# Kernel optimization log

Hardware: AMD Instinct MI355X
Metric: run time of the kernel (lower is better)

The kernel has to match this reference:

```python
import jax, jax.numpy as jnp
import numpy as np

L, E, H, FFE = 4, 512, 8, 512  # layers, embed, heads, ff dim (must equal E for residual)
HD = E // H


def _ln(x, g, b):
    mu = jnp.mean(x, -1, keepdims=True)
    var = jnp.mean((x - mu) ** 2, -1, keepdims=True)
    return (x - mu) / jnp.sqrt(var + 1e-5) * g + b


def setup_inputs() -> dict:
    key = jax.random.key(0)
    ks = jax.random.split(key, 8)
    B, S = 8, 128
    w = lambda k, shape: jax.random.normal(k, shape, jnp.float32) * 0.02
    return {
        "x": jax.random.normal(ks[0], (B, S, E), jnp.float32),
        "Wq": w(ks[1], (L, E, E)), "bq": jnp.zeros((L, E), jnp.float32),
        "Wk": w(ks[2], (L, E, E)), "bk": jnp.zeros((L, E), jnp.float32),
        "Wv": w(ks[3], (L, E, E)), "bv": jnp.zeros((L, E), jnp.float32),
        "Wo": w(ks[4], (L, E, E)), "bo": jnp.zeros((L, E), jnp.float32),
        "Wf": w(ks[5], (L, E, FFE)), "bf": jnp.zeros((L, FFE), jnp.float32),
        "g1": jnp.ones((L, E), jnp.float32), "b1": jnp.zeros((L, E), jnp.float32),
        "g2": jnp.ones((L, FFE), jnp.float32), "b2": jnp.zeros((L, FFE), jnp.float32),
    }


def reference(x, Wq, bq, Wk, bk, Wv, bv, Wo, bo, Wf, bf, g1, b1, g2, b2):
    B, S, _ = x.shape

    def stack(xb, mask):
        # xb: [B,S,E]; mask: [S] bool, True = key position inside current prefix.
        # Non-causal MHA restricted to prefix keys exactly reproduces running
        # the original stack on x[:, :s, :] (query positions beyond the prefix
        # produce values we never read).
        h = xb
        for l in range(L):
            q = (h @ Wq[l] + bq[l]).reshape(B, S, H, HD)
            k = (h @ Wk[l] + bk[l]).reshape(B, S, H, HD)
            v = (h @ Wv[l] + bv[l]).reshape(B, S, H, HD)
            sc = jnp.einsum('bqhd,bkhd->bhqk', q, k) / jnp.sqrt(jnp.float32(HD))
            sc = jnp.where(mask[None, None, None, :], sc, jnp.float32(-1e9))
            a = jax.nn.softmax(sc, axis=-1)
            o = jnp.einsum('bhqk,bkhd->bqhd', a, v).reshape(B, S, E)
            h = _ln(o @ Wo[l] + bo[l] + h, g1[l], b1[l])          # MHA + residual + LN1
            h = _ln(jax.nn.relu(h @ Wf[l] + bf[l]) + h, g2[l], b2[l])  # FF + ReLU + residual + LN2
        return h

    # masks[s-1] selects keys 0..s-1 -> prefix of length s
    masks = jnp.tril(jnp.ones((S, S), bool))
    outs = jax.vmap(stack, in_axes=(None, 0))(x, masks)  # [S, B, S, E]
    idx = jnp.arange(S)
    last = outs[idx, :, idx]  # [S, B, E]: last valid token of each prefix run
    return jnp.transpose(last, (1, 0, 2))  # [B, S, E]
```

## Files before the change

### kernel.cpp

```cpp
#include <hip/hip_runtime.h>
#include <stdint.h>

typedef unsigned short u16;
typedef __attribute__((ext_vector_type(8))) short bf16x8;
typedef __attribute__((ext_vector_type(4))) float f32x4;

#define EE 512
#define NH 8
#define HDm 64
#define SS 128
#define NB 8
#define NL 4
#define QKVW 1536

__device__ __forceinline__ float bf2f(u16 v){ union{uint32_t u; float f;} c; c.u=((uint32_t)v)<<16; return c.f; }
__device__ __forceinline__ u16 f2bf(float f){ union{float f; uint32_t u;} c; c.f=f; uint32_t u=c.u; return (u16)((u + 0x7FFFu + ((u>>16)&1u))>>16); }

__device__ __forceinline__ f32x4 mfma16(bf16x8 a, bf16x8 b, f32x4 c){
  return __builtin_amdgcn_mfma_f32_16x16x32_bf16(a,b,c,0,0,0);
}

__device__ __forceinline__ void gload16(const u16* g, u16* l){
  auto gp = reinterpret_cast<const __attribute__((address_space(1))) uint32_t*>(reinterpret_cast<uintptr_t>(g));
  auto lp = reinterpret_cast<__attribute__((address_space(3))) uint32_t*>(reinterpret_cast<uintptr_t>(l));
  __builtin_amdgcn_global_load_lds(gp, lp, 16, 0, 0);
}

#define ABAR() asm volatile("s_barrier" ::: "memory")
#define SB0()  __builtin_amdgcn_sched_barrier(0)

__device__ __forceinline__ void run_map(int bid, int cb, int U, int& r, int& u){
  int rr = 0;
  for (;;){
    int g = (cb + rr) >> 4;
    int gend = ((g + 1) << 4) - cb;
    int upr = (g + 1) * U;
    int span = (gend - rr) * upr;
    if (bid < span){ r = rr + bid / upr; u = bid % upr; return; }
    bid -= span; rr = gend;
  }
}

__global__ __launch_bounds__(256) void prep(const float* __restrict__ Wq, const float* __restrict__ Wk,
                                            const float* __restrict__ Wv, const float* __restrict__ Wo,
                                            const float* __restrict__ Wf,
                                            const float* __restrict__ bq, const float* __restrict__ bk,
                                            const float* __restrict__ bv, const float* __restrict__ x,
                                            u16* __restrict__ WqkvT, u16* __restrict__ WoT,
                                            u16* __restrict__ WfT, float* __restrict__ bqkv,
                                            u16* __restrict__ h0){
  int bid = blockIdx.x;
  int t = threadIdx.x;
  if (bid < 5120){
    __shared__ float tl[32][33];
    int grp = bid >> 10;
    int within = bid & 1023;
    int l = within >> 8, tile = within & 255;
    const float* W; u16* dst; int dstL, dstOff;
    switch(grp){
      case 0: W=Wq; dst=WqkvT; dstL=QKVW*EE; dstOff=0;    break;
      case 1: W=Wk; dst=WqkvT; dstL=QKVW*EE; dstOff=512;  break;
      case 2: W=Wv; dst=WqkvT; dstL=QKVW*EE; dstOff=1024; break;
      case 3: W=Wo; dst=WoT;   dstL=EE*EE;   dstOff=0;    break;
      default:W=Wf; dst=WfT;   dstL=EE*EE;   dstOff=0;    break;
    }
    int ot = tile & 15, it = tile >> 4;
    int c = t & 31, r = t >> 5;
    #pragma unroll
    for (int k=0;k<4;k++){
      int ri = it*32 + r + k*8;
      tl[c][r + k*8] = W[(size_t)l*262144 + (size_t)ri*512 + ot*32 + c];
    }
    __syncthreads();
    #pragma unroll
    for (int k=0;k<4;k++){
      int ro = ot*32 + r + k*8;
      dst[(size_t)l*dstL + (size_t)(dstOff + ro)*512 + it*32 + c] = f2bf(tl[r + k*8][c]);
    }
  } else if (bid < 5144){
    int i = (bid - 5120)*256 + t;
    int l = i / QKVW, n = i % QKVW;
    const float* b = (n < 512) ? bq : ((n < 1024) ? bk : bv);
    bqkv[i] = b[l*EE + (n & 511)];
  } else {
    int i = ((bid - 5144)*256 + t)*8;
    int e = i & 511;
    int pb = i >> 9;
    int b = pb & 7, pp = pb >> 3;
    const float* xp = x + (((size_t)b*SS + pp)<<9) + e;
    union{ bf16x8 v; u16 u[8]; } rv;
    #pragma unroll
    for (int j=0;j<8;j++) rv.u[j] = f2bf(xp[j]);
    *(bf16x8*)(h0 + i) = rv.v;
  }
}

template<int MODE>
__global__ __launch_bounds__(256) void gemm_bt(const u16* __restrict__ A, const u16* __restrict__ Bt,
                                               const float* __restrict__ bias, const u16* __restrict__ res,
                                               u16* __restrict__ o0, u16* __restrict__ o1, u16* __restrict__ o2,
                                               int cb, size_t res_mask){
  __shared__ u16 As[2][128*64];
  __shared__ u16 Bs[2][128*64];
  int t = threadIdx.x;
  int T = gridDim.x, NY = gridDim.y;
  int tile_idx, yb;
  if ((T & 7) == 0){
    int hw = blockIdx.y * T + blockIdx.x;
    int xcd = hw & 7, u = hw >> 3;
    yb = u % NY;
    tile_idx = (u / NY) * 8 + xcd;
  } else { tile_idx = blockIdx.x; yb = blockIdx.y; }
  size_t m0;
  if (cb < 0){
    m0 = (size_t)tile_idx * 128;
  } else {
    int r, tile; run_map(tile_idx, cb, 1, r, tile);
    m0 = (size_t)r*1024 + (size_t)tile*128;
  }
  int n0 = yb*128;
  int wid=t>>6, lane=t&63;
  int wm=wid>>1, wn=wid&1, lr=lane&15, lq=lane>>4;
  f32x4 acc[4][4] = {};
  int srow = t>>3;
  int cg2 = (t&7) ^ (srow&7);
  const u16* gA = A + (m0+(size_t)srow)*EE + cg2*8;
  const u16* gB = Bt + ((size_t)(n0+srow))*EE + cg2*8;

  auto stage = [&](int kt, int slot){
    int k0 = kt*64;
    u16* lA = As[slot] + t*8;
    u16* lB = Bs[slot] + t*8;
    #pragma unroll
    for (int j=0;j<4;j++){
      gload16(gA + (size_t)j*32*EE + k0, lA + j*2048);
      gload16(gB + (size_t)j*32*EE + k0, lB + j*2048);
    }
  };

  stage(0,0); stage(1,1);

  #pragma unroll
  for (int kt=0; kt<8; kt++){
    int slot = kt & 1;
    if (kt < 7) asm volatile("s_waitcnt vmcnt(8)" ::: "memory");
    else        asm volatile("s_waitcnt vmcnt(0)" ::: "memory");
    ABAR();
    bf16x8 a[4][2], b[4][2];
    #pragma unroll
    for (int mi=0;mi<4;mi++){
      int row = wm*64 + mi*16 + lr;
      #pragma unroll
      for (int kk=0;kk<2;kk++){
        int c = (kk*4 + lq) ^ (row&7);
        a[mi][kk] = *(const bf16x8*)(As[slot] + row*64 + c*8);
      }
    }
    #pragma unroll
    for (int ni=0;ni<4;ni++){
      int row = wn*64 + ni*16 + lr;
      #pragma unroll
      for (int kk=0;kk<2;kk++){
        int c = (kk*4 + lq) ^ (row&7);
        b[ni][kk] = *(const bf16x8*)(Bs[slot] + row*64 + c*8);
      }
    }
    asm volatile("s_waitcnt lgkmcnt(0)" ::: "memory");
    SB0();
    ABAR();
    if (kt < 6) stage(kt+2, slot);
    #pragma unroll
    for (int mi=0;mi<4;mi++)
      #pragma unroll
      for (int ni=0;ni<4;ni++){
        acc[mi][ni] = mfma16(a[mi][0], b[ni][0], acc[mi][ni]);
        acc[mi][ni] = mfma16(a[mi][1], b[ni][1], acc[mi][ni]);
      }
  }

  int g4 = lane>>4;
  u16* outp;
  int nb;
  if (MODE==0){ int sel = n0 >> 9; outp = sel==0 ? o0 : (sel==1 ? o1 : o2); nb = n0 & 511; }
  else        { outp = o0; nb = n0; }
  #pragma unroll
  for (int ni=0;ni<4;ni++){
    int coln = wn*64 + ni*16 + lr;
    float bv = bias[n0 + coln];
    int col = nb + coln;
    #pragma unroll
    for (int mi=0;mi<4;mi++){
      #pragma unroll
      for (int j=0;j<4;j++){
        size_t row = m0 + (size_t)(wm*64 + mi*16 + g4*4 + j);
        float v = acc[mi][ni][j] + bv;
        if (MODE==2) v = fmaxf(v, 0.f);
        if (MODE>=1) v += bf2f(res[(row & res_mask)*EE + col]);
        outp[row*EE + col] = f2bf(v);
      }
    }
  }
}

__global__ __launch_bounds__(256) void attn(const u16* __restrict__ Q, const u16* __restrict__ K,
                                            const u16* __restrict__ V, u16* __restrict__ Oq,
                                            int cb, int shared_qkv){
  __shared__ u16 Ks[128*72];
  __shared__ u16 Vt[64*136];
  __shared__ u16 Ps[4][16*136];
  int t = threadIdx.x;
  int idx = blockIdx.x;
  int hh = idx & 7, b = (idx>>3)&7, r = idx>>6;
  int m_run = cb + r;
  const size_t RS = (size_t)SS*NB*EE;
  size_t rbase = shared_qkv ? 0 : (size_t)r*RS;
  size_t hb = (size_t)b*EE + hh*HDm;
  size_t obase = (size_t)r*RS + hb;
  int nkc = m_run/32 + 1;
  int nkt = nkc*2;
  int nqt = m_run/16 + 1;
  int nkr = nkt*16;
  for (int i=t; i<nkr*8; i+=256){
    int row=i>>3, c=(i&7)*8;
    *(uint4*)(Ks + row*72 + c) = *(const uint4*)(K + rbase + (size_t)row*NB*EE + hb + c);
  }
  for (int i=t; i<nkr*8; i+=256){
    int row=i>>3, c=(i&7)*8;
    uint4 raw = *(const uint4*)(V + rbase + (size_t)row*NB*EE + hb + c);
    const u16* pv = (const u16*)&raw;
    #pragma unroll
    for (int j=0;j<8;j++) Vt[(c+j)*136 + row] = pv[j];
  }
  __syncthreads();
  int wid=t>>6, lane=t&63, lr=lane&15, g=lane>>4, lk=(lane>>4)*8;
  u16* Pw = Ps[wid];
  for (int iq=0; iq<2; iq++){
    int qt = wid*2 + iq;
    if (qt >= nqt) continue;
    const u16* qrow = Q + rbase + (size_t)(qt*16+lr)*NB*EE + hb;
    bf16x8 qa0 = *(const bf16x8*)(qrow + lk);
    bf16x8 qa1 = *(const bf16x8*)(qrow + 32 + lk);
    f32x4 sc[8];
    #pragma unroll
    for (int kt=0;kt<8;kt++){
      if (kt < nkt){
        f32x4 c = {};
        bf16x8 kb0 = *(const bf16x8*)(Ks + (kt*16+lr)*72 + lk);
        bf16x8 kb1 = *(const bf16x8*)(Ks + (kt*16+lr)*72 + 32 + lk);
        c = mfma16(qa0, kb0, c);
        c = mfma16(qa1, kb1, c);
        int key = kt*16 + lr;
        #pragma unroll
        for (int i2=0;i2<4;i2++)
          sc[kt][i2] = (key <= m_run) ? c[i2]*0.125f : -1e9f;
      }
    }
    #pragma unroll
    for (int i2=0;i2<4;i2++){
      float v = -3.0e38f;
      #pragma unroll
      for (int kt=0;kt<8;kt++) if (kt<nkt) v = fmaxf(v, sc[kt][i2]);
      v = fmaxf(v, __shfl_xor(v,1));
      v = fmaxf(v, __shfl_xor(v,2));
      v = fmaxf(v, __shfl_xor(v,4));
      v = fmaxf(v, __shfl_xor(v,8));
      float s = 0.f;
      #pragma unroll
      for (int kt=0;kt<8;kt++) if (kt<nkt){ float e2=__expf(sc[kt][i2]-v); sc[kt][i2]=e2; s+=e2; }
      s += __shfl_xor(s,1); s += __shfl_xor(s,2); s += __shfl_xor(s,4); s += __shfl_xor(s,8);
      float inv = 1.f/s;
      #pragma unroll
      for (int kt=0;kt<8;kt++) if (kt<nkt) sc[kt][i2] *= inv;
    }
    #pragma unroll
    for (int kt=0;kt<8;kt++) if (kt<nkt){
      #pragma unroll
      for (int i2=0;i2<4;i2++)
        Pw[(g*4+i2)*136 + kt*16 + lr] = f2bf(sc[kt][i2]);
    }
    f32x4 oa[4] = {};
    #pragma unroll
    for (int kc=0;kc<4;kc++) if (kc<nkc){
      bf16x8 pa = *(const bf16x8*)(Pw + lr*136 + kc*32 + lk);
      #pragma unroll
      for (int dt=0;dt<4;dt++){
        bf16x8 vb = *(const bf16x8*)(Vt + (dt*16+lr)*136 + kc*32 + lk);
        oa[dt] = mfma16(pa, vb, oa[dt]);
      }
    }
    #pragma unroll
    for (int dt=0;dt<4;dt++){
      #pragma unroll
      for (int j=0;j<4;j++){
        size_t prow = (size_t)(qt*16 + g*4 + j);
        Oq[obase + prow*NB*EE + dt*16 + lr] = f2bf(oa[dt][j]);
      }
    }
  }
}

__global__ __launch_bounds__(256) void lnorm(const u16* __restrict__ in, const float* __restrict__ gg,
                                             const float* __restrict__ bb, u16* __restrict__ outp,
                                             float* __restrict__ fout, int last, int cb){
  int r, u; run_map(blockIdx.x, cb, 8, r, u);
  int lane = threadIdx.x & 63;
  float gv[8], bv2[8];
  #pragma unroll
  for (int j=0;j<8;j++){ gv[j] = gg[lane*8+j]; bv2[j] = bb[lane*8+j]; }
  int m_run = cb + r;
  #pragma unroll
  for (int it=0; it<4; it++){
    int local = u*16 + it*4 + (threadIdx.x>>6);
    size_t row = (size_t)r*1024 + local;
    const u16* p = in + row*EE + lane*8;
    union{ bf16x8 v; u16 u[8]; } d; d.v = *(const bf16x8*)p;
    float f[8]; float s=0.f;
    #pragma unroll
    for (int j=0;j<8;j++){ f[j]=bf2f(d.u[j]); s+=f[j]; }
    #pragma unroll
    for (int o=1;o<64;o<<=1) s += __shfl_xor(s,o);
    float mu = s*(1.f/512.f);
    float s2=0.f;
    #pragma unroll
    for (int j=0;j<8;j++){ float tt=f[j]-mu; s2+=tt*tt; }
    #pragma unroll
    for (int o=1;o<64;o<<=1) s2 += __shfl_xor(s2,o);
    float rstd = rsqrtf(s2*(1.f/512.f)+1e-5f);
    union{ bf16x8 v; u16 u[8]; } rr;
    #pragma unroll
    for (int j=0;j<8;j++) rr.u[j] = f2bf((f[j]-mu)*rstd*gv[j] + bv2[j]);
    *(bf16x8*)(outp + row*EE + lane*8) = rr.v;
    if (last){
      int pidx = local >> 3, b3 = local & 7;
      if (pidx == m_run){
        #pragma unroll
        for (int j=0;j<8;j++) fout[((size_t)b3*SS + pidx)*EE + lane*8 + j] = bf2f(rr.u[j]);
      }
    }
  }
}

extern "C" void kernel_launch(void* const* d_in, const int* in_sizes, int n_in,
                              void* d_out, int out_size, void* d_ws, size_t ws_size,
                              hipStream_t stream){
  const float* x   = (const float*)d_in[0];
  const float* Wq  = (const float*)d_in[1];
  const float* bq  = (const float*)d_in[2];
  const float* Wk  = (const float*)d_in[3];
  const float* bk  = (const float*)d_in[4];
  const float* Wv  = (const float*)d_in[5];
  const float* bv  = (const float*)d_in[6];
  const float* Wo  = (const float*)d_in[7];
  const float* bo  = (const float*)d_in[8];
  const float* Wf  = (const float*)d_in[9];
  const float* bfb = (const float*)d_in[10];
  const float* g1  = (const float*)d_in[11];
  const float* b1  = (const float*)d_in[12];
  const float* g2  = (const float*)d_in[13];
  const float* b2  = (const float*)d_in[14];
  float* out = (float*)d_out;

  uint8_t* p = (uint8_t*)d_ws;
  u16* WqkvT = (u16*)p; p += (size_t)NL*QKVW*EE*2;
  u16* WoT   = (u16*)p; p += (size_t)NL*EE*EE*2;
  u16* WfT   = (u16*)p; p += (size_t)NL*EE*EE*2;
  float* bqkv= (float*)p; p += (size_t)NL*QKVW*4;
  u16* h0    = (u16*)p; p += (size_t)SS*NB*EE*2;
  u16* q0    = (u16*)p; p += (size_t)SS*NB*EE*2;
  u16* k0    = (u16*)p; p += (size_t)SS*NB*EE*2;
  u16* v0    = (u16*)p; p += (size_t)SS*NB*EE*2;
  size_t used = (size_t)(p - (uint8_t*)d_ws);

  int RC = 128;
  const size_t PER_RUN = (size_t)SS*NB*EE*2*5;
  while (RC > 1 && used + (size_t)RC*PER_RUN > ws_size) RC >>= 1;

  const size_t BUF = (size_t)RC*SS*NB*EE*2;
  u16* h   = (u16*)p; p += BUF;
  u16* q   = (u16*)p; p += BUF;
  u16* k   = (u16*)p; p += BUF;
  u16* v   = (u16*)p; p += BUF;
  u16* tmp = (u16*)p; p += BUF;

  const size_t NOMASK = ~(size_t)0;
  const size_t QL = (size_t)QKVW*EE;
  const size_t OL = (size_t)EE*EE;

  prep<<<5400,256,0,stream>>>(Wq, Wk, Wv, Wo, Wf, bq, bk, bv, x, WqkvT, WoT, WfT, bqkv, h0);
  gemm_bt<0><<<dim3(8,12),256,0,stream>>>(h0, WqkvT, bqkv, nullptr, q0, k0, v0, -1, 0);

  for (int cb=0; cb<SS; cb+=RC){
    int t128 = 0;
    for (int r2=0;r2<RC;r2++) t128 += (cb+r2)/16 + 1;

    attn<<<dim3(RC*64),256,0,stream>>>(q0, k0, v0, q, cb, 1);
    gemm_bt<1><<<dim3(t128,4),256,0,stream>>>(q, WoT, bo, h0, tmp, nullptr, nullptr, cb, (size_t)1023);
    lnorm<<<dim3(t128*8),256,0,stream>>>(tmp, g1, b1, h, nullptr, 0, cb);
    gemm_bt<2><<<dim3(t128,4),256,0,stream>>>(h, WfT, bfb, h, tmp, nullptr, nullptr, cb, NOMASK);
    lnorm<<<dim3(t128*8),256,0,stream>>>(tmp, g2, b2, h, nullptr, 0, cb);

    for (int l=1;l<NL;l++){
      gemm_bt<0><<<dim3(t128,12),256,0,stream>>>(h, WqkvT+(size_t)l*QL, bqkv+l*QKVW, nullptr, q, k, v, cb, 0);
      attn<<<dim3(RC*64),256,0,stream>>>(q, k, v, q, cb, 0);
      gemm_bt<1><<<dim3(t128,4),256,0,stream>>>(q, WoT+(size_t)l*OL, bo+l*EE, h, tmp, nullptr, nullptr, cb, NOMASK);
      lnorm<<<dim3(t128*8),256,0,stream>>>(tmp, g1+l*EE, b1+l*EE, h, nullptr, 0, cb);
      gemm_bt<2><<<dim3(t128,4),256,0,stream>>>(h, WfT+(size_t)l*OL, bfb+l*EE, h, tmp, nullptr, nullptr, cb, NOMASK);
      lnorm<<<dim3(t128*8),256,0,stream>>>(tmp, g2+l*EE, b2+l*EE, h, out, (l==NL-1) ? 1 : 0, cb);
    }
  }
}
```

Measured before the change: 1.832 ms.

## Fuse output/FF projection GEMMs with residual add and LayerNorm

Replaces the Wo and Wf GEMMs plus their separate LayerNorm kernels with a single kernel per stage. Each 512-thread block computes a full 64x512 row tile, reduces per-row mean and variance through shuffles and LDS, and writes the normalized bf16 rows and the final float outputs directly. This removes the tmp buffer round-trip and two launches per layer. In exchange it uses larger per-block LDS (80KB dynamic), variance computed as E[x^2]-mu^2 in fp32, and h is read as the residual and written as the output in the same kernel across different blocks' rows.

```diff
diff --git a/kernel.cpp b/kernel.cpp
--- a/kernel.cpp
+++ b/kernel.cpp
@@ -95,11 +95,10 @@
   }
 }
 
-template<int MODE>
-__global__ __launch_bounds__(256) void gemm_bt(const u16* __restrict__ A, const u16* __restrict__ Bt,
-                                               const float* __restrict__ bias, const u16* __restrict__ res,
-                                               u16* __restrict__ o0, u16* __restrict__ o1, u16* __restrict__ o2,
-                                               int cb, size_t res_mask){
+__global__ __launch_bounds__(256) void gemm_qkv(const u16* __restrict__ A, const u16* __restrict__ Bt,
+                                                const float* __restrict__ bias,
+                                                u16* __restrict__ o0, u16* __restrict__ o1, u16* __restrict__ o2,
+                                                int cb){
   __shared__ u16 As[2][128*64];
   __shared__ u16 Bs[2][128*64];
   int t = threadIdx.x;
@@ -179,10 +178,9 @@
   }
 
   int g4 = lane>>4;
-  u16* outp;
-  int nb;
-  if (MODE==0){ int sel = n0 >> 9; outp = sel==0 ? o0 : (sel==1 ? o1 : o2); nb = n0 & 511; }
-  else        { outp = o0; nb = n0; }
+  int sel = n0 >> 9;
+  u16* outp = sel==0 ? o0 : (sel==1 ? o1 : o2);
+  int nb = n0 & 511;
   #pragma unroll
   for (int ni=0;ni<4;ni++){
     int coln = wn*64 + ni*16 + lr;
@@ -193,10 +191,155 @@
       #pragma unroll
       for (int j=0;j<4;j++){
         size_t row = m0 + (size_t)(wm*64 + mi*16 + g4*4 + j);
-        float v = acc[mi][ni][j] + bv;
+        outp[row*EE + col] = f2bf(acc[mi][ni][j] + bv);
+      }
+    }
+  }
+}
+
+template<int MODE>
+__global__ __launch_bounds__(512, 2) void gemm_ln(const u16* __restrict__ A, const u16* __restrict__ Bt,
+                                                  const float* __restrict__ bias, const u16* __restrict__ res,
+                                                  size_t res_mask, const float* __restrict__ lng,
+                                                  const float* __restrict__ lnb, u16* __restrict__ outh,
+                                                  float* __restrict__ fout, int last, int cb){
+  extern __shared__ u16 lds[];
+  u16* Asl = lds;
+  u16* Bsl = lds + 8192;
+  int t = threadIdx.x;
+  int r, u64; run_map(blockIdx.x, cb, 2, r, u64);
+  int m_run = cb + r;
+  size_t m0 = (size_t)r*1024 + (size_t)u64*64;
+  int wid = t>>6, lane = t&63;
+  int lr = lane&15, lq = lane>>4;
+
+  int srow = t>>3;
+  int cg = (t&7) ^ (srow&7);
+  const u16* gA = A + (m0 + (size_t)srow)*EE + cg*8;
+  const u16* gB = Bt + (size_t)srow*EE + cg*8;
+
+  auto stageA = [&](int kt, int slot){
+    gload16(gA + kt*64, Asl + slot*4096 + t*8);
+  };
+  auto stageB = [&](int kt){
+    int k0 = kt*64;
+    #pragma unroll
+    for (int j=0;j<8;j++)
+      gload16(gB + (size_t)j*64*EE + k0, Bsl + (j*512 + t)*8);
+  };
+
+  f32x4 acc[4][4] = {};
+  stageA(0,0); stageB(0); stageA(1,1);
+
+  #pragma unroll
+  for (int kt=0; kt<8; kt++){
+    int slot = kt & 1;
+    if (kt < 7) asm volatile("s_waitcnt vmcnt(1)" ::: "memory");
+    else        asm volatile("s_waitcnt vmcnt(0)" ::: "memory");
+    ABAR();
+    bf16x8 a[4][2], b[4][2];
+    #pragma unroll
+    for (int mi=0;mi<4;mi++){
+      int row = mi*16 + lr;
+      #pragma unroll
+      for (int kk=0;kk<2;kk++){
+        int c = (kk*4 + lq) ^ (row&7);
+        a[mi][kk] = *(const bf16x8*)(Asl + slot*4096 + row*64 + c*8);
+      }
+    }
+    #pragma unroll
+    for (int ni=0;ni<4;ni++){
+      int row = wid*64 + ni*16 + lr;
+      #pragma unroll
+      for (int kk=0;kk<2;kk++){
+        int c = (kk*4 + lq) ^ (row&7);
+        b[ni][kk] = *(const bf16x8*)(Bsl + row*64 + c*8);
+      }
+    }
+    asm volatile("s_waitcnt lgkmcnt(0)" ::: "memory");
+    SB0();
+    ABAR();
+    if (kt < 7) stageB(kt+1);
+    if (kt < 6) stageA(kt+2, slot);
+    #pragma unroll
+    for (int mi=0;mi<4;mi++)
+      #pragma unroll
+      for (int ni=0;ni<4;ni++){
+        acc[mi][ni] = mfma16(a[mi][0], b[ni][0], acc[mi][ni]);
+        acc[mi][ni] = mfma16(a[mi][1], b[ni][1], acc[mi][ni]);
+      }
+  }
+
+  float psum[4][4] = {}, psq[4][4] = {};
+  #pragma unroll
+  for (int ni=0;ni<4;ni++){
+    int col = wid*64 + ni*16 + lr;
+    float bb = bias[col];
+    #pragma unroll
+    for (int mi=0;mi<4;mi++){
+      #pragma unroll
+      for (int j=0;j<4;j++){
+        size_t row = m0 + (size_t)(mi*16 + lq*4 + j);
+        float v = acc[mi][ni][j] + bb;
         if (MODE==2) v = fmaxf(v, 0.f);
-        if (MODE>=1) v += bf2f(res[(row & res_mask)*EE + col]);
-        outp[row*EE + col] = f2bf(v);
+        v += bf2f(res[(row & res_mask)*EE + col]);
+        acc[mi][ni][j] = v;
+        psum[mi][j] += v; psq[mi][j] += v*v;
+      }
+    }
+  }
+  #pragma unroll
+  for (int o=1;o<16;o<<=1){
+    #pragma unroll
+    for (int mi=0;mi<4;mi++)
+      #pragma unroll
+      for (int j=0;j<4;j++){
+        psum[mi][j] += __shfl_xor(psum[mi][j], o);
+        psq[mi][j]  += __shfl_xor(psq[mi][j], o);
+      }
+  }
+  float2* red = (float2*)lds;
+  __syncthreads();
+  if (lr == 0){
+    #pragma unroll
+    for (int mi=0;mi<4;mi++)
+      #pragma unroll
+      for (int j=0;j<4;j++)
+        red[(mi*16 + lq*4 + j)*8 + wid] = make_float2(psum[mi][j], psq[mi][j]);
+  }
+  __syncthreads();
+  float mu_[4][4], rs_[4][4];
+  #pragma unroll
+  for (int mi=0;mi<4;mi++){
+    #pragma unroll
+    for (int j=0;j<4;j++){
+      int row64 = mi*16 + lq*4 + j;
+      float sm = 0.f, sq = 0.f;
+      #pragma unroll
+      for (int k2=0;k2<8;k2++){ float2 e = red[row64*8 + k2]; sm += e.x; sq += e.y; }
+      float mu = sm * (1.f/512.f);
+      float var = sq * (1.f/512.f) - mu*mu;
+      mu_[mi][j] = mu;
+      rs_[mi][j] = rsqrtf(var + 1e-5f);
+    }
+  }
+  #pragma unroll
+  for (int ni=0;ni<4;ni++){
+    int col = wid*64 + ni*16 + lr;
+    float gg = lng[col], bb2 = lnb[col];
+    #pragma unroll
+    for (int mi=0;mi<4;mi++){
+      #pragma unroll
+      for (int j=0;j<4;j++){
+        float vv = (acc[mi][ni][j] - mu_[mi][j]) * rs_[mi][j] * gg + bb2;
+        u16 hb = f2bf(vv);
+        size_t row = m0 + (size_t)(mi*16 + lq*4 + j);
+        outh[row*EE + col] = hb;
+        if (MODE==2 && last){
+          int local = u64*64 + mi*16 + lq*4 + j;
+          int pidx = local >> 3, b3 = local & 7;
+          if (pidx == m_run) fout[((size_t)b3*SS + pidx)*EE + col] = bf2f(hb);
+        }
       }
     }
   }
@@ -299,47 +442,6 @@
   }
 }
 
-__global__ __launch_bounds__(256) void lnorm(const u16* __restrict__ in, const float* __restrict__ gg,
-                                             const float* __restrict__ bb, u16* __restrict__ outp,
-                                             float* __restrict__ fout, int last, int cb){
-  int r, u; run_map(blockIdx.x, cb, 8, r, u);
-  int lane = threadIdx.x & 63;
-  float gv[8], bv2[8];
-  #pragma unroll
-  for (int j=0;j<8;j++){ gv[j] = gg[lane*8+j]; bv2[j] = bb[lane*8+j]; }
-  int m_run = cb + r;
-  #pragma unroll
-  for (int it=0; it<4; it++){
-    int local = u*16 + it*4 + (threadIdx.x>>6);
-    size_t row = (size_t)r*1024 + local;
-    const u16* p = in + row*EE + lane*8;
-    union{ bf16x8 v; u16 u[8]; } d; d.v = *(const bf16x8*)p;
-    float f[8]; float s=0.f;
-    #pragma unroll
-    for (int j=0;j<8;j++){ f[j]=bf2f(d.u[j]); s+=f[j]; }
-    #pragma unroll
-    for (int o=1;o<64;o<<=1) s += __shfl_xor(s,o);
-    float mu = s*(1.f/512.f);
-    float s2=0.f;
-    #pragma unroll
-    for (int j=0;j<8;j++){ float tt=f[j]-mu; s2+=tt*tt; }
-    #pragma unroll
-    for (int o=1;o<64;o<<=1) s2 += __shfl_xor(s2,o);
-    float rstd = rsqrtf(s2*(1.f/512.f)+1e-5f);
-    union{ bf16x8 v; u16 u[8]; } rr;
-    #pragma unroll
-    for (int j=0;j<8;j++) rr.u[j] = f2bf((f[j]-mu)*rstd*gv[j] + bv2[j]);
-    *(bf16x8*)(outp + row*EE + lane*8) = rr.v;
-    if (last){
-      int pidx = local >> 3, b3 = local & 7;
-      if (pidx == m_run){
-        #pragma unroll
-        for (int j=0;j<8;j++) fout[((size_t)b3*SS + pidx)*EE + lane*8 + j] = bf2f(rr.u[j]);
-      }
-    }
-  }
-}
-
 extern "C" void kernel_launch(void* const* d_in, const int* in_sizes, int n_in,
                               void* d_out, int out_size, void* d_ws, size_t ws_size,
                               hipStream_t stream){
@@ -360,6 +462,9 @@
   const float* b2  = (const float*)d_in[14];
   float* out = (float*)d_out;
 
+  hipFuncSetAttribute((const void*)gemm_ln<1>, hipFuncAttributeMaxDynamicSharedMemorySize, 81920);
+  hipFuncSetAttribute((const void*)gemm_ln<2>, hipFuncAttributeMaxDynamicSharedMemorySize, 81920);
+
   uint8_t* p = (uint8_t*)d_ws;
   u16* WqkvT = (u16*)p; p += (size_t)NL*QKVW*EE*2;
   u16* WoT   = (u16*)p; p += (size_t)NL*EE*EE*2;
@@ -372,7 +477,7 @@
   size_t used = (size_t)(p - (uint8_t*)d_ws);
 
   int RC = 128;
-  const size_t PER_RUN = (size_t)SS*NB*EE*2*5;
+  const size_t PER_RUN = (size_t)SS*NB*EE*2*4;
   while (RC > 1 && used + (size_t)RC*PER_RUN > ws_size) RC >>= 1;
 
   const size_t BUF = (size_t)RC*SS*NB*EE*2;
@@ -380,32 +485,30 @@
   u16* q   = (u16*)p; p += BUF;
   u16* k   = (u16*)p; p += BUF;
   u16* v   = (u16*)p; p += BUF;
-  u16* tmp = (u16*)p; p += BUF;
 
   const size_t NOMASK = ~(size_t)0;
   const size_t QL = (size_t)QKVW*EE;
   const size_t OL = (size_t)EE*EE;
 
   prep<<<5400,256,0,stream>>>(Wq, Wk, Wv, Wo, Wf, bq, bk, bv, x, WqkvT, WoT, WfT, bqkv, h0);
-  gemm_bt<0><<<dim3(8,12),256,0,stream>>>(h0, WqkvT, bqkv, nullptr, q0, k0, v0, -1, 0);
+  gemm_qkv<<<dim3(8,12),256,0,stream>>>(h0, WqkvT, bqkv, q0, k0, v0, -1);
 
   for (int cb=0; cb<SS; cb+=RC){
     int t128 = 0;
     for (int r2=0;r2<RC;r2++) t128 += (cb+r2)/16 + 1;
+    int t64 = t128*2;
 
     attn<<<dim3(RC*64),256,0,stream>>>(q0, k0, v0, q, cb, 1);
-    gemm_bt<1><<<dim3(t128,4),256,0,stream>>>(q, WoT, bo, h0, tmp, nullptr, nullptr, cb, (size_t)1023);
-    lnorm<<<dim3(t128*8),256,0,stream>>>(tmp, g1, b1, h, nullptr, 0, cb);
-    gemm_bt<2><<<dim3(t128,4),256,0,stream>>>(h, WfT, bfb, h, tmp, nullptr, nullptr, cb, NOMASK);
-    lnorm<<<dim3(t128*8),256,0,stream>>>(tmp, g2, b2, h, nullptr, 0, cb);
+    gemm_ln<1><<<dim3(t64),512,81920,stream>>>(q, WoT, bo, h0, (size_t)1023, g1, b1, h, nullptr, 0, cb);
+    gemm_ln<2><<<dim3(t64),512,81920,stream>>>(h, WfT, bfb, h, NOMASK, g2, b2, h, nullptr, 0, cb);
 
     for (int l=1;l<NL;l++){
-      gemm_bt<0><<<dim3(t128,12),256,0,stream>>>(h, WqkvT+(size_t)l*QL, bqkv+l*QKVW, nullptr, q, k, v, cb, 0);
+      gemm_qkv<<<dim3(t128,12),256,0,stream>>>(h, WqkvT+(size_t)l*QL, bqkv+l*QKVW, q, k, v, cb);
       attn<<<dim3(RC*64),256,0,stream>>>(q, k, v, q, cb, 0);
-      gemm_bt<1><<<dim3(t128,4),256,0,stream>>>(q, WoT+(size_t)l*OL, bo+l*EE, h, tmp, nullptr, nullptr, cb, NOMASK);
-      lnorm<<<dim3(t128*8),256,0,stream>>>(tmp, g1+l*EE, b1+l*EE, h, nullptr, 0, cb);
-      gemm_bt<2><<<dim3(t128,4),256,0,stream>>>(h, WfT+(size_t)l*OL, bfb+l*EE, h, tmp, nullptr, nullptr, cb, NOMASK);
-      lnorm<<<dim3(t128*8),256,0,stream>>>(tmp, g2+l*EE, b2+l*EE, h, out, (l==NL-1) ? 1 : 0, cb);
-    }
-  }
-}
+      gemm_ln<1><<<dim3(t64),512,81920,stream>>>(q, WoT+(size_t)l*OL, bo+l*EE, h, NOMASK,
+                                                 g1+l*EE, b1+l*EE, h, nullptr, 0, cb);
+      gemm_ln<2><<<dim3(t64),512,81920,stream>>>(h, WfT+(size_t)l*OL, bfb+l*EE, h, NOMASK,
+                                                 g2+l*EE, b2+l*EE, h, out, (l==NL-1) ? 1 : 0, cb);
+    }
+  }
+}
```

Measured after the change: 2.623 ms. 1.43x slower.
